# Kernel optimization log

Hardware: AMD Instinct MI355X
Metric: run time of the kernel (lower is better)

## Reference

```python
import jax, jax.numpy as jnp
import numpy as np

NP, NA = 200000, 100000      # paper / author node counts
E = 1000000                  # edges per relation
DP, DA, H = 128, 64, 32      # paper feat, author feat, hidden


def setup_inputs() -> dict:
    key = jax.random.key(0)
    ks = jax.random.split(key, 22)
    g = lambda k, s: jax.random.normal(k, s, jnp.float32) * 0.05
    z = lambda n: jnp.zeros((n,), jnp.float32)
    return dict(
        x_paper=jax.random.normal(ks[0], (NP, DP), jnp.float32),
        x_author=jax.random.normal(ks[1], (NA, DA), jnp.float32),
        ei_cites=jax.random.randint(ks[2], (2, E), 0, NP),  # paper -> paper
        ei_writes=jnp.stack([jax.random.randint(ks[3], (E,), 0, NA),
                             jax.random.randint(ks[4], (E,), 0, NP)]),  # author -> paper
        ei_rev=jnp.stack([jax.random.randint(ks[5], (E,), 0, NP),
                          jax.random.randint(ks[6], (E,), 0, NA)]),  # paper -> author
        # layer 1 SAGEConv weights per edge type: lin_l (with bias), lin_r (no bias)
        W1l_cites=g(ks[7], (DP, H)), b1l_cites=z(H), W1r_cites=g(ks[8], (DP, H)),
        W1l_writes=g(ks[9], (DA, H)), b1l_writes=z(H), W1r_writes=g(ks[10], (DP, H)),
        W1l_rev=g(ks[11], (DP, H)), b1l_rev=z(H), W1r_rev=g(ks[12], (DA, H)),
        # layer 2
        W2l_cites=g(ks[13], (H, H)), b2l_cites=z(H), W2r_cites=g(ks[14], (H, H)),
        W2l_writes=g(ks[15], (H, H)), b2l_writes=z(H), W2r_writes=g(ks[16], (H, H)),
        W2l_rev=g(ks[17], (H, H)), b2l_rev=z(H), W2r_rev=g(ks[18], (H, H)),
        # head Linear(32, 1)
        Wh=g(ks[19], (H, 1)), bh=z(1),
    )


def _sage(x_src, x_dst, ei, Wl, bl, Wr):
    """SAGEConv: lin_l(mean_{j in N(i)} x_j) + lin_r(x_i)."""
    n_dst = x_dst.shape[0]
    src, dst = ei[0], ei[1]
    msum = jax.ops.segment_sum(x_src[src], dst, num_segments=n_dst)  # [n_dst, d_src]
    cnt = jax.ops.segment_sum(jnp.ones((ei.shape[1],), x_src.dtype), dst,
                              num_segments=n_dst)
    mean = msum / jnp.maximum(cnt, 1.0)[:, None]  # zero-degree rows stay 0
    return mean @ Wl + bl + x_dst @ Wr


def reference(x_paper, x_author, ei_cites, ei_writes, ei_rev,
              W1l_cites, b1l_cites, W1r_cites,
              W1l_writes, b1l_writes, W1r_writes,
              W1l_rev, b1l_rev, W1r_rev,
              W2l_cites, b2l_cites, W2r_cites,
              W2l_writes, b2l_writes, W2r_writes,
              W2l_rev, b2l_rev, W2r_rev,
              Wh, bh):
    # layer 1 (to_hetero: sum over edge types per dst node type), then relu
    p1 = jax.nn.relu(_sage(x_paper, x_paper, ei_cites, W1l_cites, b1l_cites, W1r_cites)
                     + _sage(x_author, x_paper, ei_writes, W1l_writes, b1l_writes, W1r_writes))
    a1 = jax.nn.relu(_sage(x_paper, x_author, ei_rev, W1l_rev, b1l_rev, W1r_rev))
    # layer 2: only the 'paper' output is consumed downstream
    p2 = (_sage(p1, p1, ei_cites, W2l_cites, b2l_cites, W2r_cites)
          + _sage(a1, p1, ei_writes, W2l_writes, b2l_writes, W2r_writes))
    # head: Linear(32, 1); model_config is None -> raw logits
    return p2 @ Wh + bh
```

## Files before the change

kernel.cpp:

```cpp
#include <hip/hip_runtime.h>
#include <hip/hip_bf16.h>


#define SPAN  2048
#define EPT   8
#define NBKT  1563
#define NPAIR 782
#define CAP   1024
#define SMASK 0x3FFFF

typedef __bf16 bf16x8 __attribute__((ext_vector_type(8)));
typedef __bf16 bf16x2 __attribute__((ext_vector_type(2)));
typedef float f32x4 __attribute__((ext_vector_type(4)));

__global__ void prep_kernel(const float* W1l_c, const float* W1l_rev,
                            const float* W1r_c, const float* W1r_w,
                            const float* W1l_w, const float* W1r_rev,
                            const float* W2l_c, const float* W2l_w,
                            const float* W2r_c, const float* W2r_w,
                            const float* b2l_c, const float* b2l_w,
                            const float* Wh, const float* bh,
                            __bf16* Bp_t, __bf16* Ba_t, float* uvec,
                            unsigned* gcur) {
    int tid = blockIdx.x * 256 + threadIdx.x;
    int nthr = gridDim.x * 256;
    for (int i = tid; i < 3 * NPAIR; i += nthr) gcur[i] = 0u;
    for (int idx = tid; idx < 96 * 128; idx += nthr) {
        int n = idx >> 7, k = idx & 127;
        float v;
        if (n < 32)      v = W1l_c[k * 32 + n];
        else if (n < 64) v = W1l_rev[k * 32 + (n - 32)];
        else             v = W1r_c[k * 32 + (n - 64)] + W1r_w[k * 32 + (n - 64)];
        Bp_t[n * 128 + k] = (__bf16)v;
    }
    for (int idx = tid; idx < 64 * 64; idx += nthr) {
        int n = idx >> 6, k = idx & 63;
        float v = (n < 32) ? W1l_w[k * 32 + n] : W1r_rev[k * 32 + (n - 32)];
        Ba_t[n * 64 + k] = (__bf16)v;
    }
    if (blockIdx.x == 0 && threadIdx.x < 32) {
        int t = threadIdx.x;
        float uc = 0.f, uw = 0.f, ur = 0.f;
        for (int j = 0; j < 32; ++j) {
            float wh = Wh[j];
            uc += W2l_c[t * 32 + j] * wh;
            uw += W2l_w[t * 32 + j] * wh;
            ur += (W2r_c[t * 32 + j] + W2r_w[t * 32 + j]) * wh;
        }
        uvec[t] = uc; uvec[32 + t] = uw; uvec[64 + t] = ur;
        if (t == 0) {
            float c0 = bh[0];
            for (int j = 0; j < 32; ++j) c0 += (b2l_c[j] + b2l_w[j]) * Wh[j];
            uvec[96] = c0;
        }
    }
}

template <int K, int NG>
__device__ __forceinline__ void proj_body(const float* __restrict__ X,
                                          const __bf16* __restrict__ Bt,
                                          __bf16* __restrict__ D0,
                                          __bf16* __restrict__ D1,
                                          __bf16* __restrict__ D2, int M, int bid) {
    constexpr int NT = NG * 2, KT = K / 32;
    int lane = threadIdx.x & 63;
    int wave = (bid * 256 + (int)threadIdx.x) >> 6;
    int m0 = wave * 16;
    if (m0 + 16 > M) return;
    int lr = lane & 15;
    int quad = lane >> 4;

    bf16x8 bfrag[NT][KT];
#pragma unroll
    for (int ct = 0; ct < NT; ++ct)
#pragma unroll
        for (int ks = 0; ks < KT; ++ks)
            bfrag[ct][ks] = *(const bf16x8*)(Bt + (ct * 16 + lr) * K + ks * 32 + quad * 8);

    bf16x8 afrag[KT];
    const float* xrow = X + (size_t)(m0 + lr) * K + quad * 8;
#pragma unroll
    for (int ks = 0; ks < KT; ++ks) {
        f32x4 lo = *(const f32x4*)(xrow + ks * 32);
        f32x4 hi = *(const f32x4*)(xrow + ks * 32 + 4);
        bf16x8 a;
#pragma unroll
        for (int j = 0; j < 4; ++j) { a[j] = (__bf16)lo[j]; a[4 + j] = (__bf16)hi[j]; }
        afrag[ks] = a;
    }

    int odd = lane & 1;
#pragma unroll
    for (int ct = 0; ct < NT; ++ct) {
        f32x4 acc = {0.f, 0.f, 0.f, 0.f};
#pragma unroll
        for (int ks = 0; ks < KT; ++ks)
            acc = __builtin_amdgcn_mfma_f32_16x16x32_bf16(afrag[ks], bfrag[ct][ks], acc, 0, 0, 0);
        __bf16* D = ((ct >> 1) == 0) ? D0 : (((ct >> 1) == 1) ? D1 : D2);
        int col = (ct & 1) * 16 + lr;
        int cw = col & ~1;
        int rbase = m0 + quad * 4;
        float o0 = __shfl_xor(acc[0], 1, 64);
        float o1 = __shfl_xor(acc[1], 1, 64);
        float o2 = __shfl_xor(acc[2], 1, 64);
        float o3 = __shfl_xor(acc[3], 1, 64);
        float s0 = odd ? o2 : acc[0], t0 = odd ? acc[2] : o0;
        float s1 = odd ? o3 : acc[1], t1 = odd ? acc[3] : o1;
        int rb = rbase + odd * 2;
        bf16x2 v0; v0[0] = (__bf16)s0; v0[1] = (__bf16)t0;
        bf16x2 v1; v1[0] = (__bf16)s1; v1[1] = (__bf16)t1;
        *(bf16x2*)(D + (size_t)(rb + 0) * 32 + cw) = v0;
        *(bf16x2*)(D + (size_t)(rb + 1) * 32 + cw) = v1;
    }
}

__device__ void scatter_body(const int* __restrict__ eiC, const int* __restrict__ eiW,
                             const int* __restrict__ eiR, unsigned* __restrict__ gcur,
                             unsigned* __restrict__ ebuf, int E, int npart, int bid,
                             unsigned* cnt) {
    int rel = bid / npart, blk = bid % npart;
    const int* ei = rel == 0 ? eiC : (rel == 1 ? eiW : eiR);
    int shift = (rel == 2) ? 6 : 7;
    unsigned dmask = (1u << shift) - 1;
    int t = threadIdx.x;
    int e0 = blk * SPAN, e1 = min(E, e0 + SPAN);
    for (int i = t; i < NPAIR; i += 256) cnt[i] = 0u;
    __syncthreads();
    int d8[EPT], s8[EPT];
#pragma unroll
    for (int j = 0; j < EPT; ++j) {
        int e = e0 + t + j * 256;
        d8[j] = (e < e1) ? ei[E + e] : -1;
        s8[j] = (e < e1) ? ei[e] : 0;
    }
#pragma unroll
    for (int j = 0; j < EPT; ++j) {
        if (d8[j] >= 0) {
            int b = d8[j] >> shift;
            atomicAdd(&cnt[b >> 1], 1u << ((b & 1) * 16));
        }
    }
    __syncthreads();
    unsigned* gp = gcur + rel * NPAIR;
    for (int i = t; i < NPAIR; i += 256) {
        unsigned c = cnt[i];
        cnt[i] = c ? atomicAdd(&gp[i], c) : 0u;
    }
    __syncthreads();
#pragma unroll
    for (int j = 0; j < EPT; ++j) {
        if (d8[j] >= 0) {
            int b = d8[j] >> shift;
            unsigned old = atomicAdd(&cnt[b >> 1], 1u << ((b & 1) * 16));
            unsigned intra = (old >> ((b & 1) * 16)) & 0xFFFFu;
            if (intra < CAP)
                ebuf[((unsigned)(rel * NBKT + b) << 10) + intra] =
                    ((unsigned)(d8[j] & dmask) << 18) | (unsigned)s8[j];
        }
    }
}

__global__ __launch_bounds__(256) void mid_kernel(
    const float* __restrict__ Xp, const float* __restrict__ Xa,
    const __bf16* __restrict__ Bp_t, const __bf16* __restrict__ Ba_t,
    __bf16* __restrict__ YpC, __bf16* __restrict__ YpR, __bf16* __restrict__ YpD,
    __bf16* __restrict__ YaW, __bf16* __restrict__ YaD,
    const int* __restrict__ eiC, const int* __restrict__ eiW,
    const int* __restrict__ eiR, unsigned* __restrict__ gcur,
    unsigned* __restrict__ ebuf, int NP, int NA, int E,
    int nPp, int nPa, int npart) {
    __shared__ unsigned cnt[NPAIR];
    int bid = blockIdx.x;
    if (bid < 3 * npart) {
        scatter_body(eiC, eiW, eiR, gcur, ebuf, E, npart, bid, cnt);
        return;
    }
    bid -= 3 * npart;
    if (bid < nPp) { proj_body<128, 3>(Xp, Bp_t, YpC, YpR, YpD, NP, bid); return; }
    bid -= nPp;
    proj_body<64, 2>(Xa, Ba_t, YaW, YaD, nullptr, NA, bid);
}

__device__ __forceinline__ void gatherCW(const __bf16* __restrict__ YA,
                                         const __bf16* __restrict__ YB,
                                         const unsigned* __restrict__ LA,
                                         const unsigned* __restrict__ LB,
                                         int oA, int nA, int oB, int nB, int l16,
                                         float2& rA, float2& rB) {
    float xA = 0.f, yA = 0.f, xB = 0.f, yB = 0.f;
    int nm = max(nA, nB);
    for (int e = 0; e < nm; e += 4) {
        unsigned a0 = (e + 0 < nA) ? LA[oA + e + 0] : 0u;
        unsigned a1 = (e + 1 < nA) ? LA[oA + e + 1] : 0u;
        unsigned a2 = (e + 2 < nA) ? LA[oA + e + 2] : 0u;
        unsigned a3 = (e + 3 < nA) ? LA[oA + e + 3] : 0u;
        unsigned b0 = (e + 0 < nB) ? LB[oB + e + 0] : 0u;
        unsigned b1 = (e + 1 < nB) ? LB[oB + e + 1] : 0u;
        unsigned b2 = (e + 2 < nB) ? LB[oB + e + 2] : 0u;
        unsigned b3 = (e + 3 < nB) ? LB[oB + e + 3] : 0u;
        bf16x2 vA0 = *(const bf16x2*)(YA + (size_t)a0 * 32 + 2 * l16);
        bf16x2 vA1 = *(const bf16x2*)(YA + (size_t)a1 * 32 + 2 * l16);
        bf16x2 vA2 = *(const bf16x2*)(YA + (size_t)a2 * 32 + 2 * l16);
        bf16x2 vA3 = *(const bf16x2*)(YA + (size_t)a3 * 32 + 2 * l16);
        bf16x2 vB0 = *(const bf16x2*)(YB + (size_t)b0 * 32 + 2 * l16);
        bf16x2 vB1 = *(const bf16x2*)(YB + (size_t)b1 * 32 + 2 * l16);
        bf16x2 vB2 = *(const bf16x2*)(YB + (size_t)b2 * 32 + 2 * l16);
        bf16x2 vB3 = *(const bf16x2*)(YB + (size_t)b3 * 32 + 2 * l16);
        if (e + 0 < nA) { xA += (float)vA0[0]; yA += (float)vA0[1]; }
        if (e + 1 < nA) { xA += (float)vA1[0]; yA += (float)vA1[1]; }
        if (e + 2 < nA) { xA += (float)vA2[0]; yA += (float)vA2[1]; }
        if (e + 3 < nA) { xA += (float)vA3[0]; yA += (float)vA3[1]; }
        if (e + 0 < nB) { xB += (float)vB0[0]; yB += (float)vB0[1]; }
        if (e + 1 < nB) { xB += (float)vB1[0]; yB += (float)vB1[1]; }
        if (e + 2 < nB) { xB += (float)vB2[0]; yB += (float)vB2[1]; }
        if (e + 3 < nB) { xB += (float)vB3[0]; yB += (float)vB3[1]; }
    }
    rA = make_float2(xA, yA);
    rB = make_float2(xB, yB);
}

__global__ __launch_bounds__(256) void sagg_kernel(
    const __bf16* __restrict__ YpC, const __bf16* __restrict__ YaW,
    const __bf16* __restrict__ YpD, const __bf16* __restrict__ YpR,
    const __bf16* __restrict__ YaD, unsigned* __restrict__ ebuf,
    const unsigned* __restrict__ gcur, int* __restrict__ nstart, int* __restrict__ ncnt,
    const float* __restrict__ b1l_c, const float* __restrict__ b1l_w,
    const float* __restrict__ b1l_r, const float* __restrict__ uvec,
    float* __restrict__ s_c, float* __restrict__ s_r, float* __restrict__ s_w,
    int NP, int NA) {
    __shared__ unsigned S0[CAP], S1[CAP];
    __shared__ int cnt0[128], exc0[128], cur0[128];
    __shared__ int cnt1[128], exc1[128], cur1[128];
    __shared__ int scan[256];
    const int NPS = NBKT * 128;
    int t = threadIdx.x;
    int sg = t >> 4, l16 = t & 15, c2 = 2 * l16;
    int bid = blockIdx.x;

    if (bid < NBKT) {
        int b = bid;
        int st0 = b << 10, st1 = (NBKT + b) << 10;
        int fsh = (b & 1) * 16;
        int n0 = min((int)((gcur[b >> 1] >> fsh) & 0xFFFFu), CAP);
        int n1 = min((int)((gcur[NPAIR + (b >> 1)] >> fsh) & 0xFFFFu), CAP);
        if (t < 128) { cnt0[t] = 0; cnt1[t] = 0; }
        __syncthreads();
        for (int i = t; i < n0; i += 256) atomicAdd(&cnt0[ebuf[st0 + i] >> 18], 1);
        for (int i = t; i < n1; i += 256) atomicAdd(&cnt1[ebuf[st1 + i] >> 18], 1);
        __syncthreads();
        int own = (t < 128) ? cnt0[t] : cnt1[t - 128];
        scan[t] = own;
        __syncthreads();
        for (int d = 1; d < 128; d <<= 1) {
            int nv = scan[t] + (((t & 127) >= d) ? scan[t - d] : 0);
            __syncthreads();
            scan[t] = nv;
            __syncthreads();
        }
        int excl = scan[t] - own;
        if (t < 128) { exc0[t] = excl; cur0[t] = excl; }
        else         { exc1[t - 128] = excl; cur1[t - 128] = excl; }
        __syncthreads();
        for (int i = t; i < n0; i += 256) {
            unsigned w = ebuf[st0 + i];
            int pos = atomicAdd(&cur0[w >> 18], 1);
            S0[pos] = w & SMASK;
        }
        for (int i = t; i < n1; i += 256) {
            unsigned w = ebuf[st1 + i];
            int pos = atomicAdd(&cur1[w >> 18], 1);
            S1[pos] = w & SMASK;
        }
        __syncthreads();
        for (int i = t; i < n0; i += 256) ebuf[st0 + i] = S0[i];
        for (int i = t; i < n1; i += 256) ebuf[st1 + i] = S1[i];
        if (t < 128) {
            nstart[b * 128 + t] = st0 + exc0[t];
            ncnt[b * 128 + t] = cnt0[t];
            nstart[NPS + b * 128 + t] = st1 + exc1[t];
            ncnt[NPS + b * 128 + t] = cnt1[t];
        }
        float u0 = uvec[c2], u1 = uvec[c2 + 1];
        float w0 = uvec[64 + c2], w1 = uvec[64 + c2 + 1];
        float bc0 = b1l_c[c2] + b1l_w[c2], bc1 = b1l_c[c2 + 1] + b1l_w[c2 + 1];
        for (int k = 0; k < 4; ++k) {
            int nd = sg * 8 + 2 * k;
            int g = b * 128 + nd;
            if (g >= NP) break;
            int nd2 = nd + 1, g2 = g + 1;
            bool v2 = (g2 < NP);
            int nC = cnt0[nd], nW = cnt1[nd];
            int nC2 = v2 ? cnt0[nd2] : 0, nW2 = v2 ? cnt1[nd2] : 0;
            float2 aC, aW, aC2, aW2;
            gatherCW(YpC, YaW, S0, S1, exc0[nd], nC, exc1[nd], nW, l16, aC, aW);
            gatherCW(YpC, YaW, S0, S1, exc0[nd2], nC2, exc1[nd2], nW2, l16, aC2, aW2);
            float rC = 1.f / (float)max(nC, 1), rW = 1.f / (float)max(nW, 1);
            bf16x2 d = *(const bf16x2*)(YpD + (size_t)g * 32 + c2);
            float p0 = fmaxf(aC.x * rC + aW.x * rW + (float)d[0] + bc0, 0.f);
            float p1 = fmaxf(aC.y * rC + aW.y * rW + (float)d[1] + bc1, 0.f);
            float vc = p0 * u0 + p1 * u1;
            float vr = p0 * w0 + p1 * w1;
            float vc2 = 0.f, vr2 = 0.f;
            if (v2) {
                float rC2 = 1.f / (float)max(nC2, 1), rW2 = 1.f / (float)max(nW2, 1);
                bf16x2 d2 = *(const bf16x2*)(YpD + (size_t)g2 * 32 + c2);
                float q0 = fmaxf(aC2.x * rC2 + aW2.x * rW2 + (float)d2[0] + bc0, 0.f);
                float q1 = fmaxf(aC2.y * rC2 + aW2.y * rW2 + (float)d2[1] + bc1, 0.f);
                vc2 = q0 * u0 + q1 * u1;
                vr2 = q0 * w0 + q1 * w1;
            }
            for (int m = 1; m < 16; m <<= 1) {
                vc += __shfl_xor(vc, m, 64);  vr += __shfl_xor(vr, m, 64);
                vc2 += __shfl_xor(vc2, m, 64); vr2 += __shfl_xor(vr2, m, 64);
            }
            if (l16 == 0) {
                s_c[g] = vc; s_r[g] = vr;
                if (v2) { s_c[g2] = vc2; s_r[g2] = vr2; }
            }
        }
    } else {
        int b = bid - NBKT;
        int st2 = (2 * NBKT + b) << 10;
        int fsh = (b & 1) * 16;
        int n2 = min((int)((gcur[2 * NPAIR + (b >> 1)] >> fsh) & 0xFFFFu), CAP);
        if (t < 128) { cnt0[t] = 0; cnt1[t] = 0; }
        __syncthreads();
        for (int i = t; i < n2; i += 256) atomicAdd(&cnt0[ebuf[st2 + i] >> 18], 1);
        __syncthreads();
        int own = (t < 128) ? cnt0[t] : 0;
        scan[t] = own;
        __syncthreads();
        for (int d = 1; d < 128; d <<= 1) {
            int nv = scan[t] + (((t & 127) >= d) ? scan[t - d] : 0);
            __syncthreads();
            scan[t] = nv;
            __syncthreads();
        }
        int excl = scan[t] - own;
        if (t < 128) { exc0[t] = excl; cur0[t] = excl; }
        __syncthreads();
        for (int i = t; i < n2; i += 256) {
            unsigned w = ebuf[st2 + i];
            int pos = atomicAdd(&cur0[w >> 18], 1);
            S0[pos] = w & SMASK;
        }
        __syncthreads();
        float uw0 = uvec[32 + c2], uw1 = uvec[32 + c2 + 1];
        float br0 = b1l_r[c2], br1 = b1l_r[c2 + 1];
        for (int k = 0; k < 2; ++k) {
            int nd = sg * 4 + 2 * k;
            int ga = b * 64 + nd;
            if (ga >= NA) break;
            int nd2 = nd + 1, ga2 = ga + 1;
            bool v2 = (ga2 < NA);
            int nR = cnt0[nd], nR2 = v2 ? cnt0[nd2] : 0;
            float2 aR, aR2;
            gatherCW(YpR, YpR, S0, S0, exc0[nd], nR, exc0[nd2], nR2, l16, aR, aR2);
            float rR = 1.f / (float)max(nR, 1);
            bf16x2 d = *(const bf16x2*)(YaD + (size_t)ga * 32 + c2);
            float p0 = fmaxf(aR.x * rR + (float)d[0] + br0, 0.f);
            float p1 = fmaxf(aR.y * rR + (float)d[1] + br1, 0.f);
            float vw = p0 * uw0 + p1 * uw1;
            float vw2 = 0.f;
            if (v2) {
                float rR2 = 1.f / (float)max(nR2, 1);
                bf16x2 d2 = *(const bf16x2*)(YaD + (size_t)ga2 * 32 + c2);
                float q0 = fmaxf(aR2.x * rR2 + (float)d2[0] + br0, 0.f);
                float q1 = fmaxf(aR2.y * rR2 + (float)d2[1] + br1, 0.f);
                vw2 = q0 * uw0 + q1 * uw1;
            }
            for (int m = 1; m < 16; m <<= 1) {
                vw += __shfl_xor(vw, m, 64); vw2 += __shfl_xor(vw2, m, 64);
            }
            if (l16 == 0) {
                s_w[ga] = vw;
                if (v2) s_w[ga2] = vw2;
            }
        }
    }
}

__global__ __launch_bounds__(256) void out_kernel(
    const float* __restrict__ s_c, const float* __restrict__ s_w,
    const float* __restrict__ s_r, const unsigned* __restrict__ ebuf,
    const int* __restrict__ nstart, const int* __restrict__ ncnt,
    const float* __restrict__ uvec, float* __restrict__ out, int NP) {
    int gn = blockIdx.x * 256 + threadIdx.x;
    if (gn >= NP) return;
    const int NPS = NBKT * 128;
    int o = nstart[gn], n = ncnt[gn];
    float sC = 0.f;
    for (int e = 0; e < n; e += 8) {
        int m = n - e;
        int a0 = ebuf[o + e];
        int a1 = (m > 1) ? (int)ebuf[o + e + 1] : a0;
        int a2 = (m > 2) ? (int)ebuf[o + e + 2] : a0;
        int a3 = (m > 3) ? (int)ebuf[o + e + 3] : a0;
        int a4 = (m > 4) ? (int)ebuf[o + e + 4] : a0;
        int a5 = (m > 5) ? (int)ebuf[o + e + 5] : a0;
        int a6 = (m > 6) ? (int)ebuf[o + e + 6] : a0;
        int a7 = (m > 7) ? (int)ebuf[o + e + 7] : a0;
        float f0 = s_c[a0], f1 = s_c[a1], f2 = s_c[a2], f3 = s_c[a3];
        float f4 = s_c[a4], f5 = s_c[a5], f6 = s_c[a6], f7 = s_c[a7];
        sC += f0;
        if (m > 1) sC += f1;
        if (m > 2) sC += f2;
        if (m > 3) sC += f3;
        if (m > 4) sC += f4;
        if (m > 5) sC += f5;
        if (m > 6) sC += f6;
        if (m > 7) sC += f7;
    }
    int o2 = nstart[NPS + gn], n2 = ncnt[NPS + gn];
    float sW = 0.f;
    for (int e = 0; e < n2; e += 8) {
        int m = n2 - e;
        int a0 = ebuf[o2 + e];
        int a1 = (m > 1) ? (int)ebuf[o2 + e + 1] : a0;
        int a2 = (m > 2) ? (int)ebuf[o2 + e + 2] : a0;
        int a3 = (m > 3) ? (int)ebuf[o2 + e + 3] : a0;
        int a4 = (m > 4) ? (int)ebuf[o2 + e + 4] : a0;
        int a5 = (m > 5) ? (int)ebuf[o2 + e + 5] : a0;
        int a6 = (m > 6) ? (int)ebuf[o2 + e + 6] : a0;
        int a7 = (m > 7) ? (int)ebuf[o2 + e + 7] : a0;
        float f0 = s_w[a0], f1 = s_w[a1], f2 = s_w[a2], f3 = s_w[a3];
        float f4 = s_w[a4], f5 = s_w[a5], f6 = s_w[a6], f7 = s_w[a7];
        sW += f0;
        if (m > 1) sW += f1;
        if (m > 2) sW += f2;
        if (m > 3) sW += f3;
        if (m > 4) sW += f4;
        if (m > 5) sW += f5;
        if (m > 6) sW += f6;
        if (m > 7) sW += f7;
    }
    out[gn] = sC / (float)max(n, 1) + sW / (float)max(n2, 1) + s_r[gn] + uvec[96];
}

extern "C" void kernel_launch(void* const* d_in, const int* in_sizes, int n_in,
                              void* d_out, int out_size, void* d_ws, size_t ws_size,
                              hipStream_t stream) {
    const float* x_paper  = (const float*)d_in[0];
    const float* x_author = (const float*)d_in[1];
    const int* eiC = (const int*)d_in[2];
    const int* eiW = (const int*)d_in[3];
    const int* eiR = (const int*)d_in[4];
    const float* W1l_c  = (const float*)d_in[5];
    const float* b1l_c  = (const float*)d_in[6];
    const float* W1r_c  = (const float*)d_in[7];
    const float* W1l_w  = (const float*)d_in[8];
    const float* b1l_w  = (const float*)d_in[9];
    const float* W1r_w  = (const float*)d_in[10];
    const float* W1l_r  = (const float*)d_in[11];
    const float* b1l_r  = (const float*)d_in[12];
    const float* W1r_r  = (const float*)d_in[13];
    const float* W2l_c  = (const float*)d_in[14];
    const float* b2l_c  = (const float*)d_in[15];
    const float* W2r_c  = (const float*)d_in[16];
    const float* W2l_w  = (const float*)d_in[17];
    const float* b2l_w  = (const float*)d_in[18];
    const float* W2r_w  = (const float*)d_in[19];
    const float* Wh = (const float*)d_in[23];
    const float* bh = (const float*)d_in[24];

    const int NP = in_sizes[0] / 128;
    const int NA = in_sizes[1] / 64;
    const int E  = in_sizes[2] / 2;
    const int npart = (E + SPAN - 1) / SPAN;
    const int nPp = (NP + 63) / 64;
    const int nPa = (NA + 63) / 64;
    const int NNODE = NBKT * 128 * 2 + NBKT * 64;

    char* p = (char*)d_ws;
    auto alloc = [&](size_t bytes) -> void* {
        void* r = (void*)p;
        p += (bytes + 255) & ~(size_t)255;
        return r;
    };
    __bf16* YpC = (__bf16*)alloc((size_t)NP * 32 * 2);
    __bf16* YpR = (__bf16*)alloc((size_t)NP * 32 * 2);
    __bf16* YpD = (__bf16*)alloc((size_t)NP * 32 * 2);
    __bf16* YaW = (__bf16*)alloc((size_t)NA * 32 * 2);
    __bf16* YaD = (__bf16*)alloc((size_t)NA * 32 * 2);
    __bf16* Bp_t = (__bf16*)alloc(96 * 128 * 2);
    __bf16* Ba_t = (__bf16*)alloc(64 * 64 * 2);
    float* uvec = (float*)alloc(128 * 4);
    float* s_c  = (float*)alloc((size_t)NP * 4);
    float* s_r  = (float*)alloc((size_t)NP * 4);
    float* s_w  = (float*)alloc((size_t)NA * 4);
    unsigned* gcur = (unsigned*)alloc((size_t)3 * NPAIR * 4);
    int* nstart = (int*)alloc((size_t)NNODE * 4);
    int* ncnt   = (int*)alloc((size_t)NNODE * 4);
    unsigned* ebuf = (unsigned*)alloc((size_t)3 * NBKT * CAP * 4);

    prep_kernel<<<20, 256, 0, stream>>>(W1l_c, W1l_r, W1r_c, W1r_w, W1l_w, W1r_r,
                                        W2l_c, W2l_w, W2r_c, W2r_w, b2l_c, b2l_w,
                                        Wh, bh, Bp_t, Ba_t, uvec, gcur);

    mid_kernel<<<nPp + nPa + 3 * npart, 256, 0, stream>>>(
        x_paper, x_author, Bp_t, Ba_t, YpC, YpR, YpD, YaW, YaD,
        eiC, eiW, eiR, gcur, ebuf, NP, NA, E, nPp, nPa, npart);

    sagg_kernel<<<2 * NBKT, 256, 0, stream>>>(
        YpC, YaW, YpD, YpR, YaD, ebuf, gcur, nstart, ncnt,
        b1l_c, b1l_w, b1l_r, uvec, s_c, s_r, s_w, NP, NA);

    out_kernel<<<(NP + 255) / 256, 256, 0, stream>>>(
        s_c, s_w, s_r, ebuf, nstart, ncnt, uvec, (float*)d_out, NP);
}
```

Baseline: 364.4 us.

## Recompute per-bucket CSR sort in out kernel instead of writing it back

The aggregation kernel no longer writes the bucket-sorted edge sources and per-node start/count arrays back to global memory. Instead, the output kernel re-reads the raw bucketed edges, recounts and re-sorts them in shared memory per 128-node bucket, and then gathers the layer-2 scalars from LDS indices. This trades global writes and reads of the sorted lists for a duplicated counting sort. It also cuts out_kernel parallelism to one 256-thread block per bucket with only 128 active threads in the gather phase.

After: 360.9 us. About the same (-1.0%).

```diff
diff --git a/kernel.cpp b/kernel.cpp
--- a/kernel.cpp
+++ b/kernel.cpp
@@ -222,8 +222,8 @@
 __global__ __launch_bounds__(256) void sagg_kernel(
     const __bf16* __restrict__ YpC, const __bf16* __restrict__ YaW,
     const __bf16* __restrict__ YpD, const __bf16* __restrict__ YpR,
-    const __bf16* __restrict__ YaD, unsigned* __restrict__ ebuf,
-    const unsigned* __restrict__ gcur, int* __restrict__ nstart, int* __restrict__ ncnt,
+    const __bf16* __restrict__ YaD, const unsigned* __restrict__ ebuf,
+    const unsigned* __restrict__ gcur,
     const float* __restrict__ b1l_c, const float* __restrict__ b1l_w,
     const float* __restrict__ b1l_r, const float* __restrict__ uvec,
     float* __restrict__ s_c, float* __restrict__ s_r, float* __restrict__ s_w,
@@ -232,7 +232,6 @@
     __shared__ int cnt0[128], exc0[128], cur0[128];
     __shared__ int cnt1[128], exc1[128], cur1[128];
     __shared__ int scan[256];
-    const int NPS = NBKT * 128;
     int t = threadIdx.x;
     int sg = t >> 4, l16 = t & 15, c2 = 2 * l16;
     int bid = blockIdx.x;
@@ -272,14 +271,6 @@
             S1[pos] = w & SMASK;
         }
         __syncthreads();
-        for (int i = t; i < n0; i += 256) ebuf[st0 + i] = S0[i];
-        for (int i = t; i < n1; i += 256) ebuf[st1 + i] = S1[i];
-        if (t < 128) {
-            nstart[b * 128 + t] = st0 + exc0[t];
-            ncnt[b * 128 + t] = cnt0[t];
-            nstart[NPS + b * 128 + t] = st1 + exc1[t];
-            ncnt[NPS + b * 128 + t] = cnt1[t];
-        }
         float u0 = uvec[c2], u1 = uvec[c2 + 1];
         float w0 = uvec[64 + c2], w1 = uvec[64 + c2 + 1];
         float bc0 = b1l_c[c2] + b1l_w[c2], bc1 = b1l_c[c2 + 1] + b1l_w[c2 + 1];
@@ -383,58 +374,100 @@
 __global__ __launch_bounds__(256) void out_kernel(
     const float* __restrict__ s_c, const float* __restrict__ s_w,
     const float* __restrict__ s_r, const unsigned* __restrict__ ebuf,
-    const int* __restrict__ nstart, const int* __restrict__ ncnt,
+    const unsigned* __restrict__ gcur,
     const float* __restrict__ uvec, float* __restrict__ out, int NP) {
-    int gn = blockIdx.x * 256 + threadIdx.x;
-    if (gn >= NP) return;
-    const int NPS = NBKT * 128;
-    int o = nstart[gn], n = ncnt[gn];
-    float sC = 0.f;
-    for (int e = 0; e < n; e += 8) {
-        int m = n - e;
-        int a0 = ebuf[o + e];
-        int a1 = (m > 1) ? (int)ebuf[o + e + 1] : a0;
-        int a2 = (m > 2) ? (int)ebuf[o + e + 2] : a0;
-        int a3 = (m > 3) ? (int)ebuf[o + e + 3] : a0;
-        int a4 = (m > 4) ? (int)ebuf[o + e + 4] : a0;
-        int a5 = (m > 5) ? (int)ebuf[o + e + 5] : a0;
-        int a6 = (m > 6) ? (int)ebuf[o + e + 6] : a0;
-        int a7 = (m > 7) ? (int)ebuf[o + e + 7] : a0;
-        float f0 = s_c[a0], f1 = s_c[a1], f2 = s_c[a2], f3 = s_c[a3];
-        float f4 = s_c[a4], f5 = s_c[a5], f6 = s_c[a6], f7 = s_c[a7];
-        sC += f0;
-        if (m > 1) sC += f1;
-        if (m > 2) sC += f2;
-        if (m > 3) sC += f3;
-        if (m > 4) sC += f4;
-        if (m > 5) sC += f5;
-        if (m > 6) sC += f6;
-        if (m > 7) sC += f7;
-    }
-    int o2 = nstart[NPS + gn], n2 = ncnt[NPS + gn];
-    float sW = 0.f;
-    for (int e = 0; e < n2; e += 8) {
-        int m = n2 - e;
-        int a0 = ebuf[o2 + e];
-        int a1 = (m > 1) ? (int)ebuf[o2 + e + 1] : a0;
-        int a2 = (m > 2) ? (int)ebuf[o2 + e + 2] : a0;
-        int a3 = (m > 3) ? (int)ebuf[o2 + e + 3] : a0;
-        int a4 = (m > 4) ? (int)ebuf[o2 + e + 4] : a0;
-        int a5 = (m > 5) ? (int)ebuf[o2 + e + 5] : a0;
-        int a6 = (m > 6) ? (int)ebuf[o2 + e + 6] : a0;
-        int a7 = (m > 7) ? (int)ebuf[o2 + e + 7] : a0;
-        float f0 = s_w[a0], f1 = s_w[a1], f2 = s_w[a2], f3 = s_w[a3];
-        float f4 = s_w[a4], f5 = s_w[a5], f6 = s_w[a6], f7 = s_w[a7];
-        sW += f0;
-        if (m > 1) sW += f1;
-        if (m > 2) sW += f2;
-        if (m > 3) sW += f3;
-        if (m > 4) sW += f4;
-        if (m > 5) sW += f5;
-        if (m > 6) sW += f6;
-        if (m > 7) sW += f7;
-    }
-    out[gn] = sC / (float)max(n, 1) + sW / (float)max(n2, 1) + s_r[gn] + uvec[96];
+    __shared__ unsigned S0[CAP], S1[CAP];
+    __shared__ int cnt0[128], exc0[128], cur0[128];
+    __shared__ int cnt1[128], exc1[128], cur1[128];
+    __shared__ int scan[256];
+    int t = threadIdx.x;
+    int b = blockIdx.x;
+    int st0 = b << 10, st1 = (NBKT + b) << 10;
+    int fsh = (b & 1) * 16;
+    int n0 = min((int)((gcur[b >> 1] >> fsh) & 0xFFFFu), CAP);
+    int n1 = min((int)((gcur[NPAIR + (b >> 1)] >> fsh) & 0xFFFFu), CAP);
+    if (t < 128) { cnt0[t] = 0; cnt1[t] = 0; }
+    __syncthreads();
+    for (int i = t; i < n0; i += 256) atomicAdd(&cnt0[ebuf[st0 + i] >> 18], 1);
+    for (int i = t; i < n1; i += 256) atomicAdd(&cnt1[ebuf[st1 + i] >> 18], 1);
+    __syncthreads();
+    int own = (t < 128) ? cnt0[t] : cnt1[t - 128];
+    scan[t] = own;
+    __syncthreads();
+    for (int d = 1; d < 128; d <<= 1) {
+        int nv = scan[t] + (((t & 127) >= d) ? scan[t - d] : 0);
+        __syncthreads();
+        scan[t] = nv;
+        __syncthreads();
+    }
+    int excl = scan[t] - own;
+    if (t < 128) { exc0[t] = excl; cur0[t] = excl; }
+    else         { exc1[t - 128] = excl; cur1[t - 128] = excl; }
+    __syncthreads();
+    for (int i = t; i < n0; i += 256) {
+        unsigned w = ebuf[st0 + i];
+        int pos = atomicAdd(&cur0[w >> 18], 1);
+        S0[pos] = w & SMASK;
+    }
+    for (int i = t; i < n1; i += 256) {
+        unsigned w = ebuf[st1 + i];
+        int pos = atomicAdd(&cur1[w >> 18], 1);
+        S1[pos] = w & SMASK;
+    }
+    __syncthreads();
+    if (t < 128) {
+        int g = b * 128 + t;
+        if (g < NP) {
+            int o = exc0[t], n = cnt0[t];
+            float sC = 0.f;
+            for (int e = 0; e < n; e += 8) {
+                int m = n - e;
+                int a0 = S0[o + e];
+                int a1 = (m > 1) ? (int)S0[o + e + 1] : a0;
+                int a2 = (m > 2) ? (int)S0[o + e + 2] : a0;
+                int a3 = (m > 3) ? (int)S0[o + e + 3] : a0;
+                int a4 = (m > 4) ? (int)S0[o + e + 4] : a0;
+                int a5 = (m > 5) ? (int)S0[o + e + 5] : a0;
+                int a6 = (m > 6) ? (int)S0[o + e + 6] : a0;
+                int a7 = (m > 7) ? (int)S0[o + e + 7] : a0;
+                float f0 = s_c[a0], f1 = s_c[a1], f2 = s_c[a2], f3 = s_c[a3];
+                float f4 = s_c[a4], f5 = s_c[a5], f6 = s_c[a6], f7 = s_c[a7];
+                sC += f0;
+                if (m > 1) sC += f1;
+                if (m > 2) sC += f2;
+                if (m > 3) sC += f3;
+                if (m > 4) sC += f4;
+                if (m > 5) sC += f5;
+                if (m > 6) sC += f6;
+                if (m > 7) sC += f7;
+            }
+            int o2 = exc1[t], n2 = cnt1[t];
+            float sW = 0.f;
+            for (int e = 0; e < n2; e += 8) {
+                int m = n2 - e;
+                int a0 = S1[o2 + e];
+                int a1 = (m > 1) ? (int)S1[o2 + e + 1] : a0;
+                int a2 = (m > 2) ? (int)S1[o2 + e + 2] : a0;
+                int a3 = (m > 3) ? (int)S1[o2 + e + 3] : a0;
+                int a4 = (m > 4) ? (int)S1[o2 + e + 4] : a0;
+                int a5 = (m > 5) ? (int)S1[o2 + e + 5] : a0;
+                int a6 = (m > 6) ? (int)S1[o2 + e + 6] : a0;
+                int a7 = (m > 7) ? (int)S1[o2 + e + 7] : a0;
+                float f0 = s_w[a0], f1 = s_w[a1], f2 = s_w[a2], f3 = s_w[a3];
+                float f4 = s_w[a4], f5 = s_w[a5], f6 = s_w[a6], f7 = s_w[a7];
+                sW += f0;
+                if (m > 1) sW += f1;
+                if (m > 2) sW += f2;
+                if (m > 3) sW += f3;
+                if (m > 4) sW += f4;
+                if (m > 5) sW += f5;
+                if (m > 6) sW += f6;
+                if (m > 7) sW += f7;
+            }
+            out[g] = sC / (float)max(n, 1) + sW / (float)max(n2, 1)
+                   + s_r[g] + uvec[96];
+        }
+    }
 }
 
 extern "C" void kernel_launch(void* const* d_in, const int* in_sizes, int n_in,
@@ -469,7 +502,6 @@
     const int npart = (E + SPAN - 1) / SPAN;
     const int nPp = (NP + 63) / 64;
     const int nPa = (NA + 63) / 64;
-    const int NNODE = NBKT * 128 * 2 + NBKT * 64;
 
     char* p = (char*)d_ws;
     auto alloc = [&](size_t bytes) -> void* {
@@ -489,8 +521,6 @@
     float* s_r  = (float*)alloc((size_t)NP * 4);
     float* s_w  = (float*)alloc((size_t)NA * 4);
     unsigned* gcur = (unsigned*)alloc((size_t)3 * NPAIR * 4);
-    int* nstart = (int*)alloc((size_t)NNODE * 4);
-    int* ncnt   = (int*)alloc((size_t)NNODE * 4);
     unsigned* ebuf = (unsigned*)alloc((size_t)3 * NBKT * CAP * 4);
 
     prep_kernel<<<20, 256, 0, stream>>>(W1l_c, W1l_r, W1r_c, W1r_w, W1l_w, W1r_r,
@@ -502,9 +532,9 @@
         eiC, eiW, eiR, gcur, ebuf, NP, NA, E, nPp, nPa, npart);
 
     sagg_kernel<<<2 * NBKT, 256, 0, stream>>>(
-        YpC, YaW, YpD, YpR, YaD, ebuf, gcur, nstart, ncnt,
+        YpC, YaW, YpD, YpR, YaD, ebuf, gcur,
         b1l_c, b1l_w, b1l_r, uvec, s_c, s_r, s_w, NP, NA);
 
-    out_kernel<<<(NP + 255) / 256, 256, 0, stream>>>(
-        s_c, s_w, s_r, ebuf, nstart, ncnt, uvec, (float*)d_out, NP);
-}
+    out_kernel<<<NBKT, 256, 0, stream>>>(
+        s_c, s_w, s_r, ebuf, gcur, uvec, (float*)d_out, NP);
+}
```
